# Optimization experiments

Hardware: AMD Instinct MI355X
Metric: run time of the kernel (lower is better)

## Reference

```python
import jax, jax.numpy as jnp
import numpy as np

N_DRUG = 50000
N_GENE = 50000
E = 600000
D_IN = 128
D_HID = 64
D_EMB = 32


def setup_inputs() -> dict:
    key = jax.random.key(0)
    ks = jax.random.split(key, 32)
    inp = {}
    inp['x_drug'] = jax.random.normal(ks[0], (N_DRUG, D_IN), jnp.float32)
    inp['x_gene'] = jax.random.normal(ks[1], (N_GENE, D_IN), jnp.float32)
    # per-etype edge lists (src,dst)
    inp['dd_src'] = jax.random.randint(ks[2], (E,), 0, N_DRUG)
    inp['dd_dst'] = jax.random.randint(ks[3], (E,), 0, N_DRUG)
    inp['dg_src'] = jax.random.randint(ks[4], (E,), 0, N_DRUG)
    inp['dg_dst'] = jax.random.randint(ks[5], (E,), 0, N_GENE)
    inp['gd_src'] = jax.random.randint(ks[6], (E,), 0, N_GENE)
    inp['gd_dst'] = jax.random.randint(ks[7], (E,), 0, N_DRUG)
    inp['gg_src'] = jax.random.randint(ks[8], (E,), 0, N_GENE)
    inp['gg_dst'] = jax.random.randint(ks[9], (E,), 0, N_GENE)
    # layer-1 per-relation weights (in -> hidden) and per-ntype biases
    s1 = 1.0 / np.sqrt(D_IN)
    inp['W1_dd'] = jax.random.normal(ks[10], (D_IN, D_HID), jnp.float32) * s1
    inp['W1_dg'] = jax.random.normal(ks[11], (D_IN, D_HID), jnp.float32) * s1
    inp['W1_gd'] = jax.random.normal(ks[12], (D_IN, D_HID), jnp.float32) * s1
    inp['W1_gg'] = jax.random.normal(ks[13], (D_IN, D_HID), jnp.float32) * s1
    inp['b1_drug'] = jnp.zeros((D_HID,), jnp.float32)
    inp['b1_gene'] = jnp.zeros((D_HID,), jnp.float32)
    # layer-2 per-relation weights (hidden -> embed) and per-ntype biases
    s2 = 1.0 / np.sqrt(D_HID)
    inp['W2_dd'] = jax.random.normal(ks[14], (D_HID, D_EMB), jnp.float32) * s2
    inp['W2_dg'] = jax.random.normal(ks[15], (D_HID, D_EMB), jnp.float32) * s2
    inp['W2_gd'] = jax.random.normal(ks[16], (D_HID, D_EMB), jnp.float32) * s2
    inp['W2_gg'] = jax.random.normal(ks[17], (D_HID, D_EMB), jnp.float32) * s2
    inp['b2_drug'] = jnp.zeros((D_EMB,), jnp.float32)
    inp['b2_gene'] = jnp.zeros((D_EMB,), jnp.float32)
    return inp


def _rel_mean(x_src, W, src, dst, n_dst):
    # transform-then-gather (efficient when out_dim <= in_dim), segment-mean over dst
    m = (x_src @ W)[src]                                  # [E, out]
    s = jax.ops.segment_sum(m, dst, num_segments=n_dst)   # [n_dst, out]
    deg = jax.ops.segment_sum(jnp.ones((src.shape[0],), m.dtype), dst, num_segments=n_dst)
    return s / jnp.maximum(deg, 1.0)[:, None]


def _rgcn_layer(xd, xg, Wdd, Wdg, Wgd, Wgg, bd, bg,
                dd_src, dd_dst, dg_src, dg_dst, gd_src, gd_dst, gg_src, gg_dst, act):
    hd = (_rel_mean(xd, Wdd, dd_src, dd_dst, N_DRUG)
          + _rel_mean(xg, Wgd, gd_src, gd_dst, N_DRUG) + bd)
    hg = (_rel_mean(xd, Wdg, dg_src, dg_dst, N_GENE)
          + _rel_mean(xg, Wgg, gg_src, gg_dst, N_GENE) + bg)
    if act:
        hd = jax.nn.relu(hd)
        hg = jax.nn.relu(hg)
    return hd, hg


def reference(x_drug, x_gene, dd_src, dd_dst, dg_src, dg_dst, gd_src, gd_dst,
              gg_src, gg_dst, W1_dd, W1_dg, W1_gd, W1_gg, b1_drug, b1_gene,
              W2_dd, W2_dg, W2_gd, W2_gg, b2_drug, b2_gene):
    hd, hg = _rgcn_layer(x_drug, x_gene, W1_dd, W1_dg, W1_gd, W1_gg, b1_drug, b1_gene,
                         dd_src, dd_dst, dg_src, dg_dst, gd_src, gd_dst, gg_src, gg_dst, True)
    hd, hg = _rgcn_layer(hd, hg, W2_dd, W2_dg, W2_gd, W2_gg, b2_drug, b2_gene,
                         dd_src, dd_dst, dg_src, dg_dst, gd_src, gd_dst, gg_src, gg_dst, False)
    # concatenate per-ntype embeddings: rows [0:N_DRUG]=drug, [N_DRUG:]=gene
    return jnp.concatenate([hd, hg], axis=0)
```

## Files before the change

kernel.cpp:

```cpp
#include <hip/hip_runtime.h>
#include <hip/hip_bf16.h>

#define N_NODE 50000
#define NEDGE  600000
#define NRANGE 128
#define RSZ    391
#define CAPB   6144
#define CHUNK  8192
#define NBLK1  74
#define GEMM_GB 196

typedef __hip_bfloat16 bf16;
typedef __attribute__((ext_vector_type(8))) short short8;
typedef __attribute__((ext_vector_type(4))) float floatx4;

__device__ __forceinline__ short f2s(float f) {
    bf16 t = __float2bfloat16(f);
    return *(short*)&t;
}
__device__ __forceinline__ unsigned pk2(float lo, float hi) {
    return ((unsigned)(unsigned short)f2s(lo)) | (((unsigned)(unsigned short)f2s(hi)) << 16);
}
__device__ __forceinline__ void acc2(float& a, float& b, unsigned w, float m) {
    a += m * __uint_as_float(w << 16);
    b += m * __uint_as_float(w & 0xFFFF0000u);
}
__device__ __forceinline__ int wscan(int x, int lane) {
#pragma unroll
    for (int d = 1; d < 64; d <<= 1) {
        int t = __shfl_up(x, d);
        if (lane >= d) x += t;
    }
    return x;
}


__global__ __launch_bounds__(512) void k_part_gemm(
    const int* __restrict__ d0, const int* __restrict__ s0,
    const int* __restrict__ d1, const int* __restrict__ s1,
    const int* __restrict__ d2, const int* __restrict__ s2,
    const int* __restrict__ d3, const int* __restrict__ s3,
    int* __restrict__ gcur, unsigned* __restrict__ gpart,
    const float* __restrict__ X0, const float* __restrict__ X1,
    const float* __restrict__ Wa0, const float* __restrict__ Wb0,
    const float* __restrict__ Wa1, const float* __restrict__ Wb1,
    bf16* __restrict__ out0, bf16* __restrict__ out1)
{
    __shared__ union {
        struct { unsigned buf[CHUNK]; int hcur[NRANGE]; int delta[NRANGE]; int wsum[2]; } p;
        short wl[4 * 8 * 512];
    } u;

    int tid = threadIdx.x;
    if (blockIdx.x < 4 * NBLK1) {
        int bid = blockIdx.x;
        int rel = bid / NBLK1;
        int c   = bid - rel * NBLK1;
        const int* dp = rel == 0 ? d0 : rel == 1 ? d1 : rel == 2 ? d2 : d3;
        const int* sp = rel == 0 ? s0 : rel == 1 ? s1 : rel == 2 ? s2 : s3;
        int e0 = c * CHUNK;
        int e1 = min(e0 + CHUNK, NEDGE);
        int cnt = e1 - e0;
        const int4* dp4 = (const int4*)(dp + e0);
        const int4* sp4 = (const int4*)(sp + e0);
        int nv = cnt >> 2;

        if (tid < NRANGE) u.p.hcur[tid] = 0;
        __syncthreads();
        for (int i = tid; i < nv; i += 512) {
            int4 d = dp4[i];
            atomicAdd(&u.p.hcur[d.x / RSZ], 1);
            atomicAdd(&u.p.hcur[d.y / RSZ], 1);
            atomicAdd(&u.p.hcur[d.z / RSZ], 1);
            atomicAdd(&u.p.hcur[d.w / RSZ], 1);
        }
        __syncthreads();
        int lane = tid & 63, wv6 = tid >> 6;
        int v = (tid < NRANGE) ? u.p.hcur[tid] : 0;
        int inc = wscan(v, lane);
        if (lane == 63 && wv6 < 2) u.p.wsum[wv6] = inc;
        __syncthreads();
        if (tid < NRANGE) {
            int incl  = inc + ((wv6 == 1) ? u.p.wsum[0] : 0);
            int start = incl - v;
            int bg    = rel * NRANGE + tid;
            int resv  = atomicAdd(&gcur[bg], v);
            u.p.delta[tid] = bg * CAPB + resv - start;
            u.p.hcur[tid]  = start;
        }
        __syncthreads();
        for (int i = tid; i < nv; i += 512) {
            int4 d = dp4[i];
            int4 s = sp4[i];
#define PUT(dd, ss) { int b = (dd) / RSZ; int p = atomicAdd(&u.p.hcur[b], 1); \
                      u.p.buf[p] = ((unsigned)b << 25) | ((unsigned)((dd) - b * RSZ) << 16) | (unsigned)(ss); }
            PUT(d.x, s.x) PUT(d.y, s.y) PUT(d.z, s.z) PUT(d.w, s.w)
#undef PUT
        }
        __syncthreads();
        for (int i = tid * 4; i < cnt; i += 2048) {
            uint4 kb = *(const uint4*)&u.p.buf[i];
            gpart[u.p.delta[kb.x >> 25] + i + 0] = kb.x;
            gpart[u.p.delta[kb.y >> 25] + i + 1] = kb.y;
            gpart[u.p.delta[kb.z >> 25] + i + 2] = kb.z;
            gpart[u.p.delta[kb.w >> 25] + i + 3] = kb.w;
        }
    } else {
        constexpr int NB = 8, KC = 4, NH = 64;
        int bid2 = blockIdx.x - 4 * NBLK1;
        int sel  = bid2 >= GEMM_GB;
        int bx   = sel ? bid2 - GEMM_GB : bid2;
        const float* X  = sel ? X1 : X0;
        const float* Wa = sel ? Wa1 : Wa0;
        const float* Wb = sel ? Wb1 : Wb0;
        bf16*       outp = sel ? out1 : out0;

        for (int i = tid; i < KC * NB * 512; i += 512) {
            int j  = i & 7;
            int n  = (i >> 3) & 15;
            int q  = (i >> 7) & 3;
            int nb = (i >> 9) & (NB - 1);
            int kc = i >> 12;
            int k  = kc * 32 + q * 8 + j;
            int c  = nb * 16 + n;
            float w = (c < NH) ? Wa[k * NH + c] : Wb[k * NH + (c - NH)];
            u.wl[i] = f2s(w);
        }
        __syncthreads();

        int lane = tid & 63, wv = tid >> 6;
        int q = lane >> 4, lidx = lane & 15;

#pragma unroll
        for (int t = 0; t < 2; t++) {
            int tile = bx * 2 + t;
            if (tile * 128 >= N_NODE) break;
            int row0 = tile * 128 + wv * 16;
            int rowA = min(row0 + lidx, N_NODE - 1);

            floatx4 acc[NB];
#pragma unroll
            for (int nb = 0; nb < NB; nb++) acc[nb] = (floatx4){0.f, 0.f, 0.f, 0.f};

#pragma unroll
            for (int kc = 0; kc < KC; kc++) {
                const float* Xf = X + (size_t)rowA * 128 + kc * 32 + q * 8;
                float4 f0 = *(const float4*)Xf;
                float4 f1 = *(const float4*)(Xf + 4);
                short8 a;
                a[0] = f2s(f0.x); a[1] = f2s(f0.y); a[2] = f2s(f0.z); a[3] = f2s(f0.w);
                a[4] = f2s(f1.x); a[5] = f2s(f1.y); a[6] = f2s(f1.z); a[7] = f2s(f1.w);
#pragma unroll
                for (int nb = 0; nb < NB; nb++) {
                    short8 b = *(const short8*)&u.wl[((kc * NB + nb) * 64 + lane) * 8];
                    acc[nb] = __builtin_amdgcn_mfma_f32_16x16x32_bf16(a, b, acc[nb], 0, 0, 0);
                }
            }
#pragma unroll
            for (int nb = 0; nb < NB; nb++) {
#pragma unroll
                for (int r = 0; r < 4; r++) {
                    int row = row0 + q * 4 + r;
                    if (row < N_NODE)
                        outp[(size_t)row * 128 + nb * 16 + lidx] = __float2bfloat16(acc[nb][r]);
                }
            }
        }
    }
}

__global__ __launch_bounds__(512) void k_csr(
    const unsigned* __restrict__ gpart, const int* __restrict__ gcnt,
    int* __restrict__ off, unsigned short* __restrict__ edges)
{
    __shared__ unsigned short stg[CAPB];
    __shared__ int cur[RSZ];
    __shared__ int wsum[8];
    int bid = blockIdx.x;
    int rel = bid >> 7, r = bid & (NRANGE - 1);
    int tid = threadIdx.x;
    int lane = tid & 63, wv = tid >> 6;
    int range0 = r * RSZ;
    int RS = min(RSZ, N_NODE - range0);
    if (RS < 0) RS = 0;
    int count = gcnt[bid];
    const uint4* gp4 = (const uint4*)(gpart + (size_t)bid * CAPB);
    const unsigned* gp = gpart + (size_t)bid * CAPB;
    int count4 = count & ~3;

    int vb = (tid < r) ? gcnt[rel * NRANGE + tid] : 0;
#pragma unroll
    for (int d = 32; d; d >>= 1) vb += __shfl_xor(vb, d);
    if (lane == 0 && wv < 2) wsum[wv] = vb;
    for (int i = tid; i < RSZ; i += 512) cur[i] = 0;
    __syncthreads();
    int base = wsum[0] + wsum[1];

    for (int i = tid * 4; i < count4; i += 2048) {
        uint4 g = gp4[i >> 2];
        atomicAdd(&cur[(g.x >> 16) & 0x1FF], 1);
        atomicAdd(&cur[(g.y >> 16) & 0x1FF], 1);
        atomicAdd(&cur[(g.z >> 16) & 0x1FF], 1);
        atomicAdd(&cur[(g.w >> 16) & 0x1FF], 1);
    }
    if (tid < (count & 3))
        atomicAdd(&cur[(gp[count4 + tid] >> 16) & 0x1FF], 1);
    __syncthreads();

    int x = (tid < RSZ) ? cur[tid] : 0;
    int inc = wscan(x, lane);
    if (lane == 63) wsum[wv] = inc;
    __syncthreads();
    int pre = 0;
#pragma unroll
    for (int w = 0; w < 7; w++) pre += (w < wv) ? wsum[w] : 0;
    int excl = inc + pre - x;
    if (tid < RSZ) cur[tid] = excl;
    __syncthreads();

    if (tid < RS)
        off[rel * (N_NODE + 1) + range0 + tid] = base + cur[tid];
    if (r == NRANGE - 1 && tid == 0) off[rel * (N_NODE + 1) + N_NODE] = NEDGE;

    for (int i = tid * 4; i < count4; i += 2048) {
        uint4 g = gp4[i >> 2];
#define SCAT(gg) { int p = atomicAdd(&cur[((gg) >> 16) & 0x1FF], 1); stg[p] = (unsigned short)((gg) & 0xFFFFu); }
        SCAT(g.x) SCAT(g.y) SCAT(g.z) SCAT(g.w)
#undef SCAT
    }
    if (tid < (count & 3)) {
        unsigned g = gp[count4 + tid];
        int p = atomicAdd(&cur[(g >> 16) & 0x1FF], 1);
        stg[p] = (unsigned short)(g & 0xFFFFu);
    }
    __syncthreads();
    for (int i = tid; i < count; i += 512)
        edges[(size_t)rel * NEDGE + base + i] = stg[i];
}

template <int K, int NOUT, bool AFP32>
__global__ __launch_bounds__(256) void k_gemm_pair(
    const void* __restrict__ X0, const void* __restrict__ X1,
    const float* __restrict__ Wa0, const float* __restrict__ Wb0,
    const float* __restrict__ Wa1, const float* __restrict__ Wb1,
    bf16* __restrict__ out0, bf16* __restrict__ out1, int M)
{
    constexpr int NB  = NOUT / 16;
    constexpr int KC  = K / 32;
    constexpr int NH  = NOUT / 2;
    constexpr int NBL = (NB == 8) ? 3 : 2;
    __shared__ short Wl[KC * NB * 512];

    int sel = blockIdx.y;
    const void*  X  = sel ? X1 : X0;
    const float* Wa = sel ? Wa1 : Wa0;
    const float* Wb = sel ? Wb1 : Wb0;
    bf16*        out = sel ? out1 : out0;

    int tid = threadIdx.x;
    for (int i = tid; i < KC * NB * 512; i += 256) {
        int j  = i & 7;
        int n  = (i >> 3) & 15;
        int q  = (i >> 7) & 3;
        int nb = (i >> 9) & (NB - 1);
        int kc = i >> (9 + NBL);
        int k  = kc * 32 + q * 8 + j;
        int c  = nb * 16 + n;
        float w = (c < NH) ? Wa[k * NH + c] : Wb[k * NH + (c - NH)];
        Wl[i] = f2s(w);
    }
    __syncthreads();

    int lane = tid & 63, wv = tid >> 6;
    int q = lane >> 4, lidx = lane & 15;
    int row0 = blockIdx.x * 64 + wv * 16;
    int rowA = min(row0 + lidx, M - 1);

    floatx4 acc[NB];
#pragma unroll
    for (int nb = 0; nb < NB; nb++) acc[nb] = (floatx4){0.f, 0.f, 0.f, 0.f};

#pragma unroll
    for (int kc = 0; kc < KC; kc++) {
        short8 a;
        if constexpr (AFP32) {
            const float* Xf = (const float*)X + (size_t)rowA * K + kc * 32 + q * 8;
            float4 f0 = *(const float4*)Xf;
            float4 f1 = *(const float4*)(Xf + 4);
            a[0] = f2s(f0.x); a[1] = f2s(f0.y); a[2] = f2s(f0.z); a[3] = f2s(f0.w);
            a[4] = f2s(f1.x); a[5] = f2s(f1.y); a[6] = f2s(f1.z); a[7] = f2s(f1.w);
        } else {
            a = *(const short8*)((const short*)X + (size_t)rowA * K + kc * 32 + q * 8);
        }
#pragma unroll
        for (int nb = 0; nb < NB; nb++) {
            short8 b = *(const short8*)&Wl[((kc * NB + nb) * 64 + lane) * 8];
            acc[nb] = __builtin_amdgcn_mfma_f32_16x16x32_bf16(a, b, acc[nb], 0, 0, 0);
        }
    }
#pragma unroll
    for (int nb = 0; nb < NB; nb++) {
#pragma unroll
        for (int r = 0; r < 4; r++) {
            int row = row0 + q * 4 + r;
            if (row < M)
                out[(size_t)row * NOUT + nb * 16 + lidx] = __float2bfloat16(acc[nb][r]);
        }
    }
}

template<int ROWU>
__device__ __forceinline__ void seg_run(
    int n, const unsigned short* __restrict__ ep, float sc,
    const unsigned* __restrict__ base, float* s)
{
    int nfull = n & ~3;
    for (int i = 0; i < nfull; i += 4) {
        int e0 = ep[i + 0];
        int e1 = ep[i + 1];
        int e2 = ep[i + 2];
        int e3 = ep[i + 3];
        uint4 w0 = *(const uint4*)(base + e0 * ROWU);
        uint4 w1 = *(const uint4*)(base + e1 * ROWU);
        uint4 w2 = *(const uint4*)(base + e2 * ROWU);
        uint4 w3 = *(const uint4*)(base + e3 * ROWU);
        acc2(s[0], s[1], w0.x, sc); acc2(s[2], s[3], w0.y, sc);
        acc2(s[4], s[5], w0.z, sc); acc2(s[6], s[7], w0.w, sc);
        acc2(s[0], s[1], w1.x, sc); acc2(s[2], s[3], w1.y, sc);
        acc2(s[4], s[5], w1.z, sc); acc2(s[6], s[7], w1.w, sc);
        acc2(s[0], s[1], w2.x, sc); acc2(s[2], s[3], w2.y, sc);
        acc2(s[4], s[5], w2.z, sc); acc2(s[6], s[7], w2.w, sc);
        acc2(s[0], s[1], w3.x, sc); acc2(s[2], s[3], w3.y, sc);
        acc2(s[4], s[5], w3.z, sc); acc2(s[6], s[7], w3.w, sc);
    }
    for (int i = nfull; i < n; i++) {
        int e = ep[i];
        uint4 w = *(const uint4*)(base + e * ROWU);
        acc2(s[0], s[1], w.x, sc); acc2(s[2], s[3], w.y, sc);
        acc2(s[4], s[5], w.z, sc); acc2(s[6], s[7], w.w, sc);
    }
}

__global__ __launch_bounds__(256) void k_gather64v5(
    const bf16* __restrict__ m1,
    const int* __restrict__ offA0, const unsigned short* __restrict__ eA0,
    const int* __restrict__ offB0, const unsigned short* __restrict__ eB0,
    const float* __restrict__ bias0, bf16* __restrict__ out0,
    const int* __restrict__ offA1, const unsigned short* __restrict__ eA1,
    const int* __restrict__ offB1, const unsigned short* __restrict__ eB1,
    const float* __restrict__ bias1, bf16* __restrict__ out1)
{
    int tid  = threadIdx.x;
    int gid  = blockIdx.x * 32 + (tid >> 3);
    int lidx = tid & 7;
    int half = (gid >= N_NODE);
    int wid  = gid - (half ? N_NODE : 0);
    const int* offA = half ? offA1 : offA0;
    const unsigned short* eA = half ? eA1 : eA0;
    const int* offB = half ? offB1 : offB0;
    const unsigned short* eB = half ? eB1 : eB0;
    const float* bias = half ? bias1 : bias0;
    bf16* out = half ? out1 : out0;

    const unsigned* base = (const unsigned*)m1 + (half ? 32 : 0) + lidx * 4;

    int begA = offA[wid], nA = offA[wid + 1] - begA;
    int begB = offB[wid], nB = offB[wid + 1] - begB;
    float ia = 1.f / (float)max(nA, 1);
    float ib = 1.f / (float)max(nB, 1);

    float s[8] = {0.f,0.f,0.f,0.f,0.f,0.f,0.f,0.f};
    seg_run<64>(nA, eA + begA, ia, base, s);
    seg_run<64>(nB, eB + begB, ib, base + N_NODE * 64, s);

    float h[8];
#pragma unroll
    for (int k = 0; k < 8; k++)
        h[k] = fmaxf(s[k] + bias[lidx * 8 + k], 0.f);
    uint4 v;
    v.x = pk2(h[0], h[1]); v.y = pk2(h[2], h[3]);
    v.z = pk2(h[4], h[5]); v.w = pk2(h[6], h[7]);
    *(uint4*)(out + (size_t)wid * 64 + lidx * 8) = v;
}

__global__ __launch_bounds__(256) void k_gather32v2(
    const bf16* __restrict__ m2,
    const int* __restrict__ offA0, const unsigned short* __restrict__ eA0,
    const int* __restrict__ offB0, const unsigned short* __restrict__ eB0,
    const float* __restrict__ bias0, float* __restrict__ out0,
    const int* __restrict__ offA1, const unsigned short* __restrict__ eA1,
    const int* __restrict__ offB1, const unsigned short* __restrict__ eB1,
    const float* __restrict__ bias1, float* __restrict__ out1)
{
    int tid  = threadIdx.x;
    int gid  = blockIdx.x * 64 + (tid >> 2);
    int lidx = tid & 3;
    if (gid >= 2 * N_NODE) return;
    int half = (gid >= N_NODE);
    int wid  = gid - (half ? N_NODE : 0);
    const int* offA = half ? offA1 : offA0;
    const unsigned short* eA = half ? eA1 : eA0;
    const int* offB = half ? offB1 : offB0;
    const unsigned short* eB = half ? eB1 : eB0;
    const float* bias = half ? bias1 : bias0;
    float* out = half ? out1 : out0;

    const unsigned* base = (const unsigned*)m2 + (half ? 16 : 0) + lidx * 4;

    int begA = offA[wid], nA = offA[wid + 1] - begA;
    int begB = offB[wid], nB = offB[wid + 1] - begB;
    float ia = 1.f / (float)max(nA, 1);
    float ib = 1.f / (float)max(nB, 1);

    float s[8] = {0.f,0.f,0.f,0.f,0.f,0.f,0.f,0.f};
    seg_run<32>(nA, eA + begA, ia, base, s);
    seg_run<32>(nB, eB + begB, ib, base + N_NODE * 32, s);

    float* o = out + (size_t)wid * 32 + lidx * 8;
    float4 v0, v1;
    v0.x = s[0] + bias[lidx * 8 + 0];
    v0.y = s[1] + bias[lidx * 8 + 1];
    v0.z = s[2] + bias[lidx * 8 + 2];
    v0.w = s[3] + bias[lidx * 8 + 3];
    v1.x = s[4] + bias[lidx * 8 + 4];
    v1.y = s[5] + bias[lidx * 8 + 5];
    v1.z = s[6] + bias[lidx * 8 + 6];
    v1.w = s[7] + bias[lidx * 8 + 7];
    *(float4*)o = v0;
    *(float4*)(o + 4) = v1;
}

extern "C" void kernel_launch(void* const* d_in, const int* in_sizes, int n_in,
                              void* d_out, int out_size, void* d_ws, size_t ws_size,
                              hipStream_t stream)
{
    const float* xd = (const float*)d_in[0];
    const float* xg = (const float*)d_in[1];
    const int* dd_src = (const int*)d_in[2];  const int* dd_dst = (const int*)d_in[3];
    const int* dg_src = (const int*)d_in[4];  const int* dg_dst = (const int*)d_in[5];
    const int* gd_src = (const int*)d_in[6];  const int* gd_dst = (const int*)d_in[7];
    const int* gg_src = (const int*)d_in[8];  const int* gg_dst = (const int*)d_in[9];
    const float* W1dd = (const float*)d_in[10];
    const float* W1dg = (const float*)d_in[11];
    const float* W1gd = (const float*)d_in[12];
    const float* W1gg = (const float*)d_in[13];
    const float* b1d  = (const float*)d_in[14];
    const float* b1g  = (const float*)d_in[15];
    const float* W2dd = (const float*)d_in[16];
    const float* W2dg = (const float*)d_in[17];
    const float* W2gd = (const float*)d_in[18];
    const float* W2gg = (const float*)d_in[19];
    const float* b2d  = (const float*)d_in[20];
    const float* b2g  = (const float*)d_in[21];
    float* out = (float*)d_out;

    int* gcur     = (int*)d_ws;
    int* off      = gcur + 512;
    unsigned short* edges = (unsigned short*)(off + 4 * (N_NODE + 1));
    bf16* md1     = (bf16*)(edges + (size_t)4 * NEDGE);
    bf16* mg1     = md1 + (size_t)N_NODE * 128;
    bf16* h       = mg1 + (size_t)N_NODE * 128;
    bf16* hd      = h;
    bf16* hg      = h + (size_t)N_NODE * 64;
    bf16* md2     = md1;
    bf16* mg2     = md1 + (size_t)N_NODE * 64;
    unsigned* gpart = (unsigned*)h;

    hipMemsetAsync(gcur, 0, 512 * sizeof(int), stream);
    k_part_gemm<<<4 * NBLK1 + 2 * GEMM_GB, 512, 0, stream>>>(
        dd_dst, dd_src, gd_dst, gd_src, dg_dst, dg_src, gg_dst, gg_src, gcur, gpart,
        xd, xg, W1dd, W1dg, W1gd, W1gg, md1, mg1);

    k_csr<<<512, 512, 0, stream>>>(gpart, gcur, off, edges);

    const int* off_dd = off + 0 * (N_NODE + 1);
    const int* off_gd = off + 1 * (N_NODE + 1);
    const int* off_dg = off + 2 * (N_NODE + 1);
    const int* off_gg = off + 3 * (N_NODE + 1);
    const unsigned short* e_dd = edges + (size_t)0 * NEDGE;
    const unsigned short* e_gd = edges + (size_t)1 * NEDGE;
    const unsigned short* e_dg = edges + (size_t)2 * NEDGE;
    const unsigned short* e_gg = edges + (size_t)3 * NEDGE;

    int g64_grid = (2 * N_NODE) / 32;
    int g32_grid = (2 * N_NODE + 63) / 64;
    dim3 gemm2_grid((N_NODE + 63) / 64, 2);

    k_gather64v5<<<g64_grid, 256, 0, stream>>>(
        md1,
        off_dd, e_dd, off_gd, e_gd, b1d, hd,
        off_dg, e_dg, off_gg, e_gg, b1g, hg);

    k_gemm_pair<64, 64, false><<<gemm2_grid, 256, 0, stream>>>(
        hd, hg, W2dd, W2dg, W2gd, W2gg, md2, mg2, N_NODE);

    k_gather32v2<<<g32_grid, 256, 0, stream>>>(
        md2,
        off_dd, e_dd, off_gd, e_gd, b2d, out,
        off_dg, e_dg, off_gg, e_gg, b2g, out + (size_t)N_NODE * 32);
}
```

Baseline: 289.7 us.

## Move layer-1 GEMM blocks from partition kernel into CSR kernel, halve partition chunk

The layer-1 feature GEMM blocks now run alongside the CSR-building kernel instead of the edge-partitioning kernel. The partition kernel becomes standalone with half-size chunks, which doubles its block count. The aim is to balance work across the two kernels and give the partition step more parallelism. The cost is more global atomic reservations and smaller per-block batches in the partition step.

Measured after the change: 304.5 us. 1.05x slower.

```diff
diff --git a/kernel.cpp b/kernel.cpp
--- a/kernel.cpp
+++ b/kernel.cpp
@@ -6,9 +6,10 @@
 #define NRANGE 128
 #define RSZ    391
 #define CAPB   6144
-#define CHUNK  8192
-#define NBLK1  74
+#define CHUNK  4096
+#define NBLK1  147
 #define GEMM_GB 196
+#define NCSR   512
 
 typedef __hip_bfloat16 bf16;
 typedef __attribute__((ext_vector_type(8))) short short8;
@@ -35,79 +36,151 @@
 }
 
 
-__global__ __launch_bounds__(512) void k_part_gemm(
+__global__ __launch_bounds__(512) void k_part(
     const int* __restrict__ d0, const int* __restrict__ s0,
     const int* __restrict__ d1, const int* __restrict__ s1,
     const int* __restrict__ d2, const int* __restrict__ s2,
     const int* __restrict__ d3, const int* __restrict__ s3,
-    int* __restrict__ gcur, unsigned* __restrict__ gpart,
+    int* __restrict__ gcur, unsigned* __restrict__ gpart)
+{
+    __shared__ unsigned buf[CHUNK];
+    __shared__ int hcur[NRANGE];
+    __shared__ int delta[NRANGE];
+    __shared__ int wsum2[2];
+
+    int tid = threadIdx.x;
+    int bid = blockIdx.x;
+    int rel = bid / NBLK1;
+    int c   = bid - rel * NBLK1;
+    const int* dp = rel == 0 ? d0 : rel == 1 ? d1 : rel == 2 ? d2 : d3;
+    const int* sp = rel == 0 ? s0 : rel == 1 ? s1 : rel == 2 ? s2 : s3;
+    int e0 = c * CHUNK;
+    int e1 = min(e0 + CHUNK, NEDGE);
+    int cnt = e1 - e0;
+    const int4* dp4 = (const int4*)(dp + e0);
+    const int4* sp4 = (const int4*)(sp + e0);
+    int nv = cnt >> 2;
+
+    if (tid < NRANGE) hcur[tid] = 0;
+    __syncthreads();
+    for (int i = tid; i < nv; i += 512) {
+        int4 d = dp4[i];
+        atomicAdd(&hcur[d.x / RSZ], 1);
+        atomicAdd(&hcur[d.y / RSZ], 1);
+        atomicAdd(&hcur[d.z / RSZ], 1);
+        atomicAdd(&hcur[d.w / RSZ], 1);
+    }
+    __syncthreads();
+    int lane = tid & 63, wv6 = tid >> 6;
+    int v = (tid < NRANGE) ? hcur[tid] : 0;
+    int inc = wscan(v, lane);
+    if (lane == 63 && wv6 < 2) wsum2[wv6] = inc;
+    __syncthreads();
+    if (tid < NRANGE) {
+        int incl  = inc + ((wv6 == 1) ? wsum2[0] : 0);
+        int start = incl - v;
+        int bg    = rel * NRANGE + tid;
+        int resv  = atomicAdd(&gcur[bg], v);
+        delta[tid] = bg * CAPB + resv - start;
+        hcur[tid]  = start;
+    }
+    __syncthreads();
+    for (int i = tid; i < nv; i += 512) {
+        int4 d = dp4[i];
+        int4 s = sp4[i];
+#define PUT(dd, ss) { int b = (dd) / RSZ; int p = atomicAdd(&hcur[b], 1); \
+                      buf[p] = ((unsigned)b << 25) | ((unsigned)((dd) - b * RSZ) << 16) | (unsigned)(ss); }
+        PUT(d.x, s.x) PUT(d.y, s.y) PUT(d.z, s.z) PUT(d.w, s.w)
+#undef PUT
+    }
+    __syncthreads();
+    for (int i = tid * 4; i < cnt; i += 2048) {
+        uint4 kb = *(const uint4*)&buf[i];
+        gpart[delta[kb.x >> 25] + i + 0] = kb.x;
+        gpart[delta[kb.y >> 25] + i + 1] = kb.y;
+        gpart[delta[kb.z >> 25] + i + 2] = kb.z;
+        gpart[delta[kb.w >> 25] + i + 3] = kb.w;
+    }
+}
+
+__global__ __launch_bounds__(512) void k_csr_gemm(
+    const unsigned* __restrict__ gpart, const int* __restrict__ gcnt,
+    int* __restrict__ off, unsigned short* __restrict__ edges,
     const float* __restrict__ X0, const float* __restrict__ X1,
     const float* __restrict__ Wa0, const float* __restrict__ Wb0,
     const float* __restrict__ Wa1, const float* __restrict__ Wb1,
     bf16* __restrict__ out0, bf16* __restrict__ out1)
 {
     __shared__ union {
-        struct { unsigned buf[CHUNK]; int hcur[NRANGE]; int delta[NRANGE]; int wsum[2]; } p;
+        struct { unsigned short stg[CAPB]; int cur[RSZ]; int wsum[8]; } c;
         short wl[4 * 8 * 512];
     } u;
 
     int tid = threadIdx.x;
-    if (blockIdx.x < 4 * NBLK1) {
+    if (blockIdx.x < NCSR) {
         int bid = blockIdx.x;
-        int rel = bid / NBLK1;
-        int c   = bid - rel * NBLK1;
-        const int* dp = rel == 0 ? d0 : rel == 1 ? d1 : rel == 2 ? d2 : d3;
-        const int* sp = rel == 0 ? s0 : rel == 1 ? s1 : rel == 2 ? s2 : s3;
-        int e0 = c * CHUNK;
-        int e1 = min(e0 + CHUNK, NEDGE);
-        int cnt = e1 - e0;
-        const int4* dp4 = (const int4*)(dp + e0);
-        const int4* sp4 = (const int4*)(sp + e0);
-        int nv = cnt >> 2;
-
-        if (tid < NRANGE) u.p.hcur[tid] = 0;
+        int rel = bid >> 7, r = bid & (NRANGE - 1);
+        int lane = tid & 63, wv = tid >> 6;
+        int range0 = r * RSZ;
+        int RS = min(RSZ, N_NODE - range0);
+        if (RS < 0) RS = 0;
+        int count = gcnt[bid];
+        const uint4* gp4 = (const uint4*)(gpart + (size_t)bid * CAPB);
+        const unsigned* gp = gpart + (size_t)bid * CAPB;
+        int count4 = count & ~3;
+
+        int vb = (tid < r) ? gcnt[rel * NRANGE + tid] : 0;
+#pragma unroll
+        for (int d = 32; d; d >>= 1) vb += __shfl_xor(vb, d);
+        if (lane == 0 && wv < 2) u.c.wsum[wv] = vb;
+        for (int i = tid; i < RSZ; i += 512) u.c.cur[i] = 0;
         __syncthreads();
-        for (int i = tid; i < nv; i += 512) {
-            int4 d = dp4[i];
-            atomicAdd(&u.p.hcur[d.x / RSZ], 1);
-            atomicAdd(&u.p.hcur[d.y / RSZ], 1);
-            atomicAdd(&u.p.hcur[d.z / RSZ], 1);
-            atomicAdd(&u.p.hcur[d.w / RSZ], 1);
-        }
+        int base = u.c.wsum[0] + u.c.wsum[1];
+
+        for (int i = tid * 4; i < count4; i += 2048) {
+            uint4 g = gp4[i >> 2];
+            atomicAdd(&u.c.cur[(g.x >> 16) & 0x1FF], 1);
+            atomicAdd(&u.c.cur[(g.y >> 16) & 0x1FF], 1);
+            atomicAdd(&u.c.cur[(g.z >> 16) & 0x1FF], 1);
+            atomicAdd(&u.c.cur[(g.w >> 16) & 0x1FF], 1);
+        }
+        if (tid < (count & 3))
+            atomicAdd(&u.c.cur[(gp[count4 + tid] >> 16) & 0x1FF], 1);
         __syncthreads();
-        int lane = tid & 63, wv6 = tid >> 6;
-        int v = (tid < NRANGE) ? u.p.hcur[tid] : 0;
-        int inc = wscan(v, lane);
-        if (lane == 63 && wv6 < 2) u.p.wsum[wv6] = inc;
+
+        int x = (tid < RSZ) ? u.c.cur[tid] : 0;
+        int inc = wscan(x, lane);
+        if (lane == 63) u.c.wsum[wv] = inc;
         __syncthreads();
-        if (tid < NRANGE) {
-            int incl  = inc + ((wv6 == 1) ? u.p.wsum[0] : 0);
-            int start = incl - v;
-            int bg    = rel * NRANGE + tid;
-            int resv  = atomicAdd(&gcur[bg], v);
-            u.p.delta[tid] = bg * CAPB + resv - start;
-            u.p.hcur[tid]  = start;
-        }
+        int pre = 0;
+#pragma unroll
+        for (int w = 0; w < 7; w++) pre += (w < wv) ? u.c.wsum[w] : 0;
+        int excl = inc + pre - x;
+        if (tid < RSZ) u.c.cur[tid] = excl;
         __syncthreads();
-        for (int i = tid; i < nv; i += 512) {
-            int4 d = dp4[i];
-            int4 s = sp4[i];
-#define PUT(dd, ss) { int b = (dd) / RSZ; int p = atomicAdd(&u.p.hcur[b], 1); \
-                      u.p.buf[p] = ((unsigned)b << 25) | ((unsigned)((dd) - b * RSZ) << 16) | (unsigned)(ss); }
-            PUT(d.x, s.x) PUT(d.y, s.y) PUT(d.z, s.z) PUT(d.w, s.w)
-#undef PUT
+
+        if (tid < RS)
+            off[rel * (N_NODE + 1) + range0 + tid] = base + u.c.cur[tid];
+        if (r == NRANGE - 1 && tid == 0) off[rel * (N_NODE + 1) + N_NODE] = NEDGE;
+
+        for (int i = tid * 4; i < count4; i += 2048) {
+            uint4 g = gp4[i >> 2];
+#define SCAT(gg) { int p = atomicAdd(&u.c.cur[((gg) >> 16) & 0x1FF], 1); \
+                   u.c.stg[p] = (unsigned short)((gg) & 0xFFFFu); }
+            SCAT(g.x) SCAT(g.y) SCAT(g.z) SCAT(g.w)
+#undef SCAT
+        }
+        if (tid < (count & 3)) {
+            unsigned g = gp[count4 + tid];
+            int p = atomicAdd(&u.c.cur[(g >> 16) & 0x1FF], 1);
+            u.c.stg[p] = (unsigned short)(g & 0xFFFFu);
         }
         __syncthreads();
-        for (int i = tid * 4; i < cnt; i += 2048) {
-            uint4 kb = *(const uint4*)&u.p.buf[i];
-            gpart[u.p.delta[kb.x >> 25] + i + 0] = kb.x;
-            gpart[u.p.delta[kb.y >> 25] + i + 1] = kb.y;
-            gpart[u.p.delta[kb.z >> 25] + i + 2] = kb.z;
-            gpart[u.p.delta[kb.w >> 25] + i + 3] = kb.w;
-        }
+        for (int i = tid; i < count; i += 512)
+            edges[(size_t)rel * NEDGE + base + i] = u.c.stg[i];
     } else {
         constexpr int NB = 8, KC = 4, NH = 64;
-        int bid2 = blockIdx.x - 4 * NBLK1;
+        int bid2 = blockIdx.x - NCSR;
         int sel  = bid2 >= GEMM_GB;
         int bx   = sel ? bid2 - GEMM_GB : bid2;
         const float* X  = sel ? X1 : X0;
@@ -167,75 +240,6 @@
             }
         }
     }
-}
-
-__global__ __launch_bounds__(512) void k_csr(
-    const unsigned* __restrict__ gpart, const int* __restrict__ gcnt,
-    int* __restrict__ off, unsigned short* __restrict__ edges)
-{
-    __shared__ unsigned short stg[CAPB];
-    __shared__ int cur[RSZ];
-    __shared__ int wsum[8];
-    int bid = blockIdx.x;
-    int rel = bid >> 7, r = bid & (NRANGE - 1);
-    int tid = threadIdx.x;
-    int lane = tid & 63, wv = tid >> 6;
-    int range0 = r * RSZ;
-    int RS = min(RSZ, N_NODE - range0);
-    if (RS < 0) RS = 0;
-    int count = gcnt[bid];
-    const uint4* gp4 = (const uint4*)(gpart + (size_t)bid * CAPB);
-    const unsigned* gp = gpart + (size_t)bid * CAPB;
-    int count4 = count & ~3;
-
-    int vb = (tid < r) ? gcnt[rel * NRANGE + tid] : 0;
-#pragma unroll
-    for (int d = 32; d; d >>= 1) vb += __shfl_xor(vb, d);
-    if (lane == 0 && wv < 2) wsum[wv] = vb;
-    for (int i = tid; i < RSZ; i += 512) cur[i] = 0;
-    __syncthreads();
-    int base = wsum[0] + wsum[1];
-
-    for (int i = tid * 4; i < count4; i += 2048) {
-        uint4 g = gp4[i >> 2];
-        atomicAdd(&cur[(g.x >> 16) & 0x1FF], 1);
-        atomicAdd(&cur[(g.y >> 16) & 0x1FF], 1);
-        atomicAdd(&cur[(g.z >> 16) & 0x1FF], 1);
-        atomicAdd(&cur[(g.w >> 16) & 0x1FF], 1);
-    }
-    if (tid < (count & 3))
-        atomicAdd(&cur[(gp[count4 + tid] >> 16) & 0x1FF], 1);
-    __syncthreads();
-
-    int x = (tid < RSZ) ? cur[tid] : 0;
-    int inc = wscan(x, lane);
-    if (lane == 63) wsum[wv] = inc;
-    __syncthreads();
-    int pre = 0;
-#pragma unroll
-    for (int w = 0; w < 7; w++) pre += (w < wv) ? wsum[w] : 0;
-    int excl = inc + pre - x;
-    if (tid < RSZ) cur[tid] = excl;
-    __syncthreads();
-
-    if (tid < RS)
-        off[rel * (N_NODE + 1) + range0 + tid] = base + cur[tid];
-    if (r == NRANGE - 1 && tid == 0) off[rel * (N_NODE + 1) + N_NODE] = NEDGE;
-
-    for (int i = tid * 4; i < count4; i += 2048) {
-        uint4 g = gp4[i >> 2];
-#define SCAT(gg) { int p = atomicAdd(&cur[((gg) >> 16) & 0x1FF], 1); stg[p] = (unsigned short)((gg) & 0xFFFFu); }
-        SCAT(g.x) SCAT(g.y) SCAT(g.z) SCAT(g.w)
-#undef SCAT
-    }
-    if (tid < (count & 3)) {
-        unsigned g = gp[count4 + tid];
-        int p = atomicAdd(&cur[(g >> 16) & 0x1FF], 1);
-        stg[p] = (unsigned short)(g & 0xFFFFu);
-    }
-    __syncthreads();
-    for (int i = tid; i < count; i += 512)
-        edges[(size_t)rel * NEDGE + base + i] = stg[i];
 }
 
 template <int K, int NOUT, bool AFP32>
@@ -467,11 +471,12 @@
     unsigned* gpart = (unsigned*)h;
 
     hipMemsetAsync(gcur, 0, 512 * sizeof(int), stream);
-    k_part_gemm<<<4 * NBLK1 + 2 * GEMM_GB, 512, 0, stream>>>(
-        dd_dst, dd_src, gd_dst, gd_src, dg_dst, dg_src, gg_dst, gg_src, gcur, gpart,
+    k_part<<<4 * NBLK1, 512, 0, stream>>>(
+        dd_dst, dd_src, gd_dst, gd_src, dg_dst, dg_src, gg_dst, gg_src, gcur, gpart);
+
+    k_csr_gemm<<<NCSR + 2 * GEMM_GB, 512, 0, stream>>>(
+        gpart, gcur, off, edges,
         xd, xg, W1dd, W1dg, W1gd, W1gg, md1, mg1);
-
-    k_csr<<<512, 512, 0, stream>>>(gpart, gcur, off, edges);
 
     const int* off_dd = off + 0 * (N_NODE + 1);
     const int* off_gd = off + 1 * (N_NODE + 1);
```
